# Optimization experiments

Hardware: AMD Instinct MI355X
Metric: run time of the kernel (lower is better)

Reference implementation:

```python
import jax, jax.numpy as jnp
import numpy as np

SPARSITY = 0.1  # fraction of entries kept (set to 1)


def _subnet(scores, k):
    # Mirrors GetSubnet.forward: full sort of flattened |scores|, zero the
    # lowest j = int((1-k)*n) ranks, set the rest to 1 (ties broken by sort order).
    flat = scores.ravel()
    n = flat.size
    j = int((1.0 - k) * n)  # static python int
    order = jnp.argsort(flat)  # ascending
    out = jnp.zeros((n,), dtype=scores.dtype).at[order[j:]].set(1)
    return out.reshape(scores.shape)


def setup_inputs() -> dict:
    key = jax.random.key(0)
    kA, kB = jax.random.split(key)
    # kaiming_uniform_(a=sqrt(5)) => U(-bound, bound), bound = sqrt(6/((1+5)*fan_in)) = 1/sqrt(fan_in)
    A_shape = (1024, 16384)
    B_shape = (16384, 1024)
    bA = 1.0 / np.sqrt(A_shape[1])
    bB = 1.0 / np.sqrt(B_shape[1])
    lora_A_mask = jax.random.uniform(kA, A_shape, jnp.float32, -bA, bA)
    lora_B_mask = jax.random.uniform(kB, B_shape, jnp.float32, -bB, bB)
    return {"lora_A_mask": lora_A_mask, "lora_B_mask": lora_B_mask}


def reference(lora_A_mask, lora_B_mask):
    mask_A = _subnet(jnp.abs(lora_A_mask), SPARSITY)
    mask_B = _subnet(jnp.abs(lora_B_mask), SPARSITY)
    return (mask_A, mask_B)
```

## Files before the change

kernel.cpp:

```cpp
#include <hip/hip_runtime.h>
#include <stdint.h>


#define NBINS       65536u
#define HWORDS      (2u * NBINS)
#define CCAP        65536u
#define TOTAL_WORDS 33554432u
#define RWORDS      (2u * CCAP * 2u)
#define RBASE       (TOTAL_WORDS - RWORDS)
#define SKIP_WORD   (RBASE - 16777216u)
#define SKIP_F4     (SKIP_WORD / 4u)
#define CNT(m)      (32u + (uint32_t)(m) * 16u)
#define LCAP        256u

typedef float floatx4 __attribute__((ext_vector_type(4)));

__device__ __forceinline__ void nt_store4(float4* p, float a, float b, float c, float d) {
  floatx4 v = {a, b, c, d};
  __builtin_nontemporal_store(v, reinterpret_cast<floatx4*>(p));
}

__global__ void init_k(uint32_t* __restrict__ ws, uint32_t* __restrict__ outbuf) {
  uint32_t i = blockIdx.x * blockDim.x + threadIdx.x;
  if (i < HWORDS) outbuf[i] = 0u;
  if (i < 64u) ws[i] = 0u;
}

__global__ __launch_bounds__(1024, 1) void hist_k(const float* __restrict__ A,
                                                  const float* __restrict__ B,
                                                  uint32_t* __restrict__ outbuf,
                                                  int nvec) {
  const int m = blockIdx.y;
  const float4* __restrict__ src = (const float4*)(m == 0 ? A : B);
  uint32_t* gh = outbuf + (uint32_t)m * NBINS;
  __shared__ uint32_t h[NBINS / 2];
  for (int i = threadIdx.x; i < (int)(NBINS / 2); i += blockDim.x) h[i] = 0u;
  __syncthreads();
  int idx0 = blockIdx.x * blockDim.x + threadIdx.x;
  int stride = gridDim.x * blockDim.x;
  for (int i = idx0; i < nvec; i += stride) {
    float4 f = src[i];
    const float v[4] = {f.x, f.y, f.z, f.w};
#pragma unroll
    for (int c = 0; c < 4; c++) {
      uint32_t u = __float_as_uint(v[c]) & 0x7fffffffu;
      uint32_t b = u >> 15;
      atomicAdd(&h[b >> 1], 1u << ((b & 1u) * 16u));
    }
  }
  __syncthreads();
  for (int w = threadIdx.x; w < (int)(NBINS / 2); w += blockDim.x) {
    uint32_t x = h[w];
    uint32_t c0 = x & 0xffffu, c1 = x >> 16;
    if (c0) atomicAdd(&gh[2 * w], c0);
    if (c1) atomicAdd(&gh[2 * w + 1], c1);
  }
}

__global__ __launch_bounds__(1024, 1) void scan16_k(const uint32_t* __restrict__ outbuf,
                                                    uint32_t* __restrict__ ws, uint32_t j) {
  const int m = blockIdx.x;
  const uint32_t* gh = outbuf + (uint32_t)m * NBINS;
  uint32_t* W = ws + m * 8;
  __shared__ uint32_t csum[1024];
  __shared__ uint32_t ps[1024];
  __shared__ uint32_t sChunk, sRank;
  __shared__ uint32_t bins[64];
  const int t = threadIdx.x;
  const int w = t >> 6, l = t & 63;
  for (int k = 0; k < 64; k++) {
    uint32_t v = gh[(w << 12) + (k << 6) + l];
#pragma unroll
    for (int off = 32; off; off >>= 1) v += __shfl_xor(v, off, 64);
    if (l == 0) csum[(w << 6) + k] = v;
  }
  __syncthreads();
  ps[t] = csum[t];
  __syncthreads();
  for (int off = 1; off < 1024; off <<= 1) {
    uint32_t v = (t >= off) ? ps[t - off] : 0u;
    __syncthreads();
    ps[t] += v;
    __syncthreads();
  }
  uint32_t base = (t == 0) ? 0u : ps[t - 1];
  if (j >= base && j < base + csum[t]) { sChunk = (uint32_t)t; sRank = j - base; }
  __syncthreads();
  const uint32_t chunk = sChunk, rk = sRank;
  if (t < 64) bins[t] = gh[chunk * 64u + (uint32_t)t];
  __syncthreads();
  if (t < 64) {
    uint32_t lt = 0u;
    for (int k2 = 0; k2 < t; k2++) lt += bins[k2];
    if (rk >= lt && rk < lt + bins[t]) { W[0] = chunk * 64u + (uint32_t)t; W[1] = rk - lt; }
  }
}

__global__ void mask_collect_k(const float* __restrict__ A, const float* __restrict__ B,
                               float* __restrict__ out, uint32_t* __restrict__ ws,
                               uint32_t* __restrict__ outbuf, int nvec, int n) {
  const int m = blockIdx.y;
  const float4* __restrict__ src = (const float4*)(m == 0 ? A : B);
  float4* __restrict__ dst = (float4*)(out + (size_t)m * (size_t)n);
  const uint32_t P = ws[m * 8];
  uint32_t* cand = outbuf + RBASE + (uint32_t)m * (CCAP * 2u);
  __shared__ uint32_t lbuf[2u * LCAP];
  __shared__ uint32_t ln, lbase;
  if (threadIdx.x == 0) ln = 0u;
  __syncthreads();
  const int i0 = blockIdx.x * blockDim.x + threadIdx.x;
  const int S = gridDim.x * blockDim.x;
  float4 f[4];
#pragma unroll
  for (int q = 0; q < 4; q++) {
    int i = i0 + q * S;
    if (i < nvec) f[q] = src[i];
  }
#pragma unroll
  for (int q = 0; q < 4; q++) {
    int i = i0 + q * S;
    if (i >= nvec) break;
    const float v[4] = {f[q].x, f[q].y, f[q].z, f[q].w};
    float r[4];
#pragma unroll
    for (int c = 0; c < 4; c++) {
      uint32_t u = __float_as_uint(v[c]) & 0x7fffffffu;
      uint32_t p = u >> 15;
      r[c] = (p > P) ? 1.0f : 0.0f;
      if (p == P) {
        uint32_t s = atomicAdd(&ln, 1u);
        if (s < LCAP) { lbuf[2u * s] = (uint32_t)i * 4u + (uint32_t)c; lbuf[2u * s + 1u] = u; }
      }
    }
    if (!(m == 1 && i >= (int)SKIP_F4))
      nt_store4(&dst[i], r[0], r[1], r[2], r[3]);
  }
  __syncthreads();
  uint32_t c = ln; if (c > LCAP) c = LCAP;
  if (threadIdx.x == 0 && c) lbase = atomicAdd(&ws[CNT(m)], c);
  __syncthreads();
  for (uint32_t t = threadIdx.x; t < c; t += blockDim.x) {
    uint32_t g = lbase + t;
    if (g < CCAP) { cand[2u * g] = lbuf[2u * t]; cand[2u * g + 1u] = lbuf[2u * t + 1u]; }
  }
}

__global__ __launch_bounds__(1024, 1) void select_fix_k(uint32_t* __restrict__ ws,
                                                        uint32_t* __restrict__ outbuf,
                                                        float* __restrict__ out, int n) {
  const int m = blockIdx.x;
  uint32_t* W = ws + m * 8;
  const uint32_t* cand = outbuf + RBASE + (uint32_t)m * (CCAP * 2u);
  __shared__ uint32_t h[32768];
  __shared__ uint32_t ps[1024];
  __shared__ uint32_t sT, sTarget, sC;
  __shared__ uint32_t tie_idx[1024];
  __shared__ uint32_t tie_n;
  const int t = threadIdx.x;
  uint32_t nc = ws[CNT(m)]; if (nc > CCAP) nc = CCAP;
  const uint32_t r = W[1];
  const uint32_t P = W[0];
  if (t == 0) { tie_n = 0u; sT = P << 15; sTarget = 0u; sC = 0u; }
  for (int i = t; i < 32768; i += 1024) h[i] = 0u;
  __syncthreads();
  for (uint32_t e = t; e < nc; e += 1024u)
    atomicAdd(&h[cand[2u * e + 1u] & 32767u], 1u);
  __syncthreads();
  uint32_t s = 0u;
  for (int k = 0; k < 32; k++) s += h[t * 32 + k];
  ps[t] = s;
  __syncthreads();
  for (int off = 1; off < 1024; off <<= 1) {
    uint32_t v = (t >= off) ? ps[t - off] : 0u;
    __syncthreads();
    ps[t] += v;
    __syncthreads();
  }
  uint32_t base = (t == 0) ? 0u : ps[t - 1];
  for (int k = 0; k < 32; k++) {
    uint32_t b = (uint32_t)t * 32u + (uint32_t)k;
    uint32_t c = h[b];
    if (r >= base && r < base + c) { sT = (P << 15) | b; sTarget = r - base; }
    base += c;
  }
  __syncthreads();
  const uint32_t T = sT, target = sTarget;
  for (uint32_t e = t; e < nc; e += 1024u) {
    if (cand[2u * e + 1u] == T) {
      uint32_t slot = atomicAdd(&tie_n, 1u);
      if (slot < 1024u) tie_idx[slot] = cand[2u * e];
    }
  }
  __syncthreads();
  uint32_t E2 = tie_n; if (E2 > 1024u) E2 = 1024u;
  for (uint32_t c2 = t; c2 < E2; c2 += 1024u) {
    uint32_t xi = tie_idx[c2];
    uint32_t lt = 0u;
    for (uint32_t k2 = 0; k2 < E2; k2++) lt += (tie_idx[k2] < xi) ? 1u : 0u;
    if (lt == target) sC = xi;
  }
  __syncthreads();
  if (t == 0) { W[3] = T; W[4] = sC; }
  const uint32_t C = sC;
  float* dstf = out + (size_t)m * (size_t)n;
  for (uint32_t e = t; e < nc; e += 1024u) {
    uint32_t idx = cand[2u * e];
    if (m == 1 && idx >= SKIP_WORD) continue;
    uint32_t u = cand[2u * e + 1u];
    dstf[idx] = (u > T || (u == T && idx >= C)) ? 1.0f : 0.0f;
  }
}

__global__ void fill_tail_k(const float* __restrict__ B, float* __restrict__ out,
                            const uint32_t* __restrict__ ws, int n) {
  const uint32_t* W = ws + 8;
  const uint32_t T = W[3], C = W[4];
  const float4* __restrict__ src = (const float4*)B;
  float4* __restrict__ dst = (float4*)(out + (size_t)n);
  uint32_t i = SKIP_F4 + blockIdx.x * blockDim.x + threadIdx.x;
  if (i < (uint32_t)(n / 4)) {
    float4 f = src[i];
    const float v[4] = {f.x, f.y, f.z, f.w};
    float r[4];
#pragma unroll
    for (int c = 0; c < 4; c++) {
      uint32_t u = __float_as_uint(v[c]) & 0x7fffffffu;
      uint32_t idx = i * 4u + (uint32_t)c;
      r[c] = (u > T || (u == T && idx >= C)) ? 1.0f : 0.0f;
    }
    nt_store4(&dst[i], r[0], r[1], r[2], r[3]);
  }
}

extern "C" void kernel_launch(void* const* d_in, const int* in_sizes, int n_in,
                              void* d_out, int out_size, void* d_ws, size_t ws_size,
                              hipStream_t stream) {
  const float* A = (const float*)d_in[0];
  const float* B = (const float*)d_in[1];
  float* out = (float*)d_out;
  uint32_t* ws = (uint32_t*)d_ws;
  uint32_t* outbuf = (uint32_t*)d_out;
  const int n = in_sizes[0];
  const int nvec = n / 4;
  const uint32_t j = (uint32_t)((1.0 - 0.1) * (double)n);

  init_k<<<(HWORDS + 255) / 256, 256, 0, stream>>>(ws, outbuf);
  hist_k<<<dim3(128, 2), 1024, 0, stream>>>(A, B, outbuf, nvec);
  scan16_k<<<2, 1024, 0, stream>>>(outbuf, ws, j);
  mask_collect_k<<<dim3(4096, 2), 256, 0, stream>>>(A, B, out, ws, outbuf, nvec, n);
  select_fix_k<<<2, 1024, 0, stream>>>(ws, outbuf, out, n);
  fill_tail_k<<<(n / 4 - SKIP_F4 + 255) / 256, 256, 0, stream>>>(B, out, ws, n);
}
```

Measured before the change: 413.4 us.

## Fuse radix-select pipeline into one cooperative persistent kernel with grid syncs

Replaces the six-kernel launch sequence with a single cooperative kernel that runs init, histogram, scan, mask/collect, tie-fix and tail-fill phases separated by grid.sync, sized to one 1024-thread block per CU (capped at 256 blocks). It aims to remove launch gaps and inter-kernel drains, and enlarges the per-block candidate buffer because each block now covers far more elements. The fused path uses regular stores instead of nontemporal stores, and has far fewer blocks for the bandwidth-heavy passes, so there is less memory-level parallelism. The old kernels stay as a fallback if the cooperative launch fails.

```diff
diff --git a/kernel.cpp b/kernel.cpp
--- a/kernel.cpp
+++ b/kernel.cpp
@@ -1,9 +1,11 @@
 #include <hip/hip_runtime.h>
+#include <hip/hip_cooperative_groups.h>
 #include <stdint.h>
 
+namespace cg = cooperative_groups;
+
 
 #define NBINS       65536u
-#define HWORDS      (2u * NBINS)
 #define CCAP        65536u
 #define TOTAL_WORDS 33554432u
 #define RWORDS      (2u * CCAP * 2u)
@@ -11,18 +13,233 @@
 #define SKIP_WORD   (RBASE - 16777216u)
 #define SKIP_F4     (SKIP_WORD / 4u)
 #define CNT(m)      (32u + (uint32_t)(m) * 16u)
-#define LCAP        256u
+#define TPB         1024
+#define LCAP        2048u
+#define SMW         34824
 
 typedef float floatx4 __attribute__((ext_vector_type(4)));
-
 __device__ __forceinline__ void nt_store4(float4* p, float a, float b, float c, float d) {
   floatx4 v = {a, b, c, d};
   __builtin_nontemporal_store(v, reinterpret_cast<floatx4*>(p));
 }
+__device__ __forceinline__ uint32_t agent_ld(const uint32_t* p) {
+  return __hip_atomic_load(p, __ATOMIC_RELAXED, __HIP_MEMORY_SCOPE_AGENT);
+}
+
+__global__ __launch_bounds__(1024, 1) void fused_k(
+    const float* __restrict__ A, const float* __restrict__ B,
+    float* __restrict__ out, uint32_t* __restrict__ ws,
+    int nvec, int n, uint32_t j)
+{
+  __shared__ uint32_t smem[SMW];
+  cg::grid_group grid = cg::this_grid();
+  const int nblk = (int)gridDim.x;
+  const int nbm  = nblk >> 1;
+  const int blk  = (int)blockIdx.x;
+  const int t    = (int)threadIdx.x;
+  uint32_t* outu = (uint32_t*)out;
+  const int m  = (blk >= nbm) ? 1 : 0;
+  const int bb = blk - m * nbm;
+  const int S  = nbm * TPB;
+
+  for (uint32_t i = (uint32_t)blk * TPB + t; i < 2u * NBINS; i += (uint32_t)nblk * TPB)
+    outu[i] = 0u;
+  if (blk == 0 && t < 64) ws[t] = 0u;
+  __threadfence();
+  grid.sync();
+
+  {
+    const float4* __restrict__ src = (const float4*)(m == 0 ? A : B);
+    uint32_t* gh = outu + (uint32_t)m * NBINS;
+    for (int i2 = t; i2 < 32768; i2 += TPB) smem[i2] = 0u;
+    __syncthreads();
+    for (int i = bb * TPB + t; i < nvec; i += S) {
+      float4 f = src[i];
+      const float v[4] = {f.x, f.y, f.z, f.w};
+#pragma unroll
+      for (int c = 0; c < 4; c++) {
+        uint32_t u = __float_as_uint(v[c]) & 0x7fffffffu;
+        uint32_t bin = u >> 15;
+        atomicAdd(&smem[bin >> 1], 1u << ((bin & 1u) * 16u));
+      }
+    }
+    __syncthreads();
+    for (int w = t; w < 32768; w += TPB) {
+      uint32_t x = smem[w];
+      uint32_t c0 = x & 0xffffu, c1 = x >> 16;
+      if (c0) atomicAdd(&gh[2 * w], c0);
+      if (c1) atomicAdd(&gh[2 * w + 1], c1);
+    }
+  }
+  __threadfence();
+  grid.sync();
+
+  if (blk < 2) {
+    const int mm = blk;
+    const uint32_t* gh = outu + (uint32_t)mm * NBINS;
+    uint32_t* bins = smem;
+    uint32_t* csum = smem + 32768;
+    uint32_t* ps   = smem + 33792;
+    const int w = t >> 6, l = t & 63;
+    for (int k = 0; k < 64; k++) {
+      uint32_t v = gh[(w << 12) + (k << 6) + l];
+#pragma unroll
+      for (int off = 32; off; off >>= 1) v += __shfl_xor(v, off, 64);
+      if (l == 0) csum[(w << 6) + k] = v;
+    }
+    __syncthreads();
+    ps[t] = csum[t];
+    __syncthreads();
+    for (int off = 1; off < 1024; off <<= 1) {
+      uint32_t v = (t >= off) ? ps[t - off] : 0u;
+      __syncthreads();
+      ps[t] += v;
+      __syncthreads();
+    }
+    uint32_t base = (t == 0) ? 0u : ps[t - 1];
+    if (j >= base && j < base + csum[t]) { smem[34816] = (uint32_t)t; smem[34817] = j - base; }
+    __syncthreads();
+    const uint32_t chunk = smem[34816], rk = smem[34817];
+    if (t < 64) bins[t] = gh[chunk * 64u + (uint32_t)t];
+    __syncthreads();
+    if (t < 64) {
+      uint32_t lt = 0u;
+      for (int k2 = 0; k2 < t; k2++) lt += bins[k2];
+      if (rk >= lt && rk < lt + bins[t]) {
+        ws[mm * 8] = chunk * 64u + (uint32_t)t;
+        ws[mm * 8 + 1] = rk - lt;
+      }
+    }
+  }
+  __threadfence();
+  grid.sync();
+
+  {
+    const float4* __restrict__ src = (const float4*)(m == 0 ? A : B);
+    float4* __restrict__ dst = (float4*)(out + (size_t)m * (size_t)n);
+    uint32_t* cand = outu + RBASE + (uint32_t)m * (CCAP * 2u);
+    uint32_t* lbuf = smem;
+    const uint32_t P = agent_ld(&ws[m * 8]);
+    if (t == 0) smem[34816] = 0u;
+    __syncthreads();
+    for (int i = bb * TPB + t; i < nvec; i += S) {
+      float4 f = src[i];
+      const float v[4] = {f.x, f.y, f.z, f.w};
+      float r[4];
+#pragma unroll
+      for (int c = 0; c < 4; c++) {
+        uint32_t u = __float_as_uint(v[c]) & 0x7fffffffu;
+        uint32_t p = u >> 15;
+        r[c] = (p > P) ? 1.0f : 0.0f;
+        if (p == P) {
+          uint32_t s = atomicAdd(&smem[34816], 1u);
+          if (s < LCAP) { lbuf[2u * s] = (uint32_t)i * 4u + (uint32_t)c; lbuf[2u * s + 1u] = u; }
+        }
+      }
+      if (!(m == 1 && i >= (int)SKIP_F4))
+        dst[i] = make_float4(r[0], r[1], r[2], r[3]);
+    }
+    __syncthreads();
+    uint32_t c = smem[34816]; if (c > LCAP) c = LCAP;
+    if (t == 0 && c) smem[34817] = atomicAdd(&ws[CNT(m)], c);
+    __syncthreads();
+    if (c) {
+      const uint32_t gb = smem[34817];
+      for (uint32_t e = t; e < c; e += TPB) {
+        uint32_t g = gb + e;
+        if (g < CCAP) { cand[2u * g] = lbuf[2u * e]; cand[2u * g + 1u] = lbuf[2u * e + 1u]; }
+      }
+    }
+  }
+  __threadfence();
+  grid.sync();
+
+  if (blk < 2) {
+    const int mm = blk;
+    uint32_t* W = ws + mm * 8;
+    const uint32_t* cand = outu + RBASE + (uint32_t)mm * (CCAP * 2u);
+    uint32_t* h   = smem;
+    uint32_t* ps  = smem + 32768;
+    uint32_t* tie = smem + 33792;
+    uint32_t nc = agent_ld(&ws[CNT(mm)]); if (nc > CCAP) nc = CCAP;
+    const uint32_t r = agent_ld(&W[1]);
+    const uint32_t P = agent_ld(&W[0]);
+    if (t == 0) { smem[34816] = 0u; smem[34817] = P << 15; smem[34818] = 0u; smem[34819] = 0u; }
+    for (int i2 = t; i2 < 32768; i2 += TPB) h[i2] = 0u;
+    __syncthreads();
+    for (uint32_t e = t; e < nc; e += TPB)
+      atomicAdd(&h[cand[2u * e + 1u] & 32767u], 1u);
+    __syncthreads();
+    uint32_t s = 0u;
+    for (int k = 0; k < 32; k++) s += h[t * 32 + k];
+    ps[t] = s;
+    __syncthreads();
+    for (int off = 1; off < 1024; off <<= 1) {
+      uint32_t v = (t >= off) ? ps[t - off] : 0u;
+      __syncthreads();
+      ps[t] += v;
+      __syncthreads();
+    }
+    uint32_t base = (t == 0) ? 0u : ps[t - 1];
+    for (int k = 0; k < 32; k++) {
+      uint32_t b2 = (uint32_t)t * 32u + (uint32_t)k;
+      uint32_t c2 = h[b2];
+      if (r >= base && r < base + c2) { smem[34817] = (P << 15) | b2; smem[34818] = r - base; }
+      base += c2;
+    }
+    __syncthreads();
+    const uint32_t T = smem[34817], target = smem[34818];
+    for (uint32_t e = t; e < nc; e += TPB) {
+      if (cand[2u * e + 1u] == T) {
+        uint32_t slot = atomicAdd(&smem[34816], 1u);
+        if (slot < 1024u) tie[slot] = cand[2u * e];
+      }
+    }
+    __syncthreads();
+    uint32_t E2 = smem[34816]; if (E2 > 1024u) E2 = 1024u;
+    for (uint32_t c2 = t; c2 < E2; c2 += TPB) {
+      uint32_t xi = tie[c2];
+      uint32_t lt = 0u;
+      for (uint32_t k2 = 0; k2 < E2; k2++) lt += (tie[k2] < xi) ? 1u : 0u;
+      if (lt == target) smem[34819] = xi;
+    }
+    __syncthreads();
+    if (t == 0) { W[3] = T; W[4] = smem[34819]; }
+    const uint32_t C = smem[34819];
+    float* dstf = out + (size_t)mm * (size_t)n;
+    for (uint32_t e = t; e < nc; e += TPB) {
+      uint32_t idx = cand[2u * e];
+      if (mm == 1 && idx >= SKIP_WORD) continue;
+      uint32_t u = cand[2u * e + 1u];
+      dstf[idx] = (u > T || (u == T && idx >= C)) ? 1.0f : 0.0f;
+    }
+  }
+  __threadfence();
+  grid.sync();
+
+  {
+    const uint32_t T = agent_ld(&ws[8 + 3]), C = agent_ld(&ws[8 + 4]);
+    for (uint32_t tid = (uint32_t)blk * TPB + t; tid < RWORDS / 4u; tid += (uint32_t)nblk * TPB) {
+      uint32_t i = SKIP_F4 + tid;
+      float4 f = ((const float4*)B)[i];
+      const float v[4] = {f.x, f.y, f.z, f.w};
+      float r[4];
+#pragma unroll
+      for (int c = 0; c < 4; c++) {
+        uint32_t u = __float_as_uint(v[c]) & 0x7fffffffu;
+        uint32_t idx = i * 4u + (uint32_t)c;
+        r[c] = (u > T || (u == T && idx >= C)) ? 1.0f : 0.0f;
+      }
+      ((float4*)(out + (size_t)n))[i] = make_float4(r[0], r[1], r[2], r[3]);
+    }
+  }
+}
+
+#define FLCAP 256u
 
 __global__ void init_k(uint32_t* __restrict__ ws, uint32_t* __restrict__ outbuf) {
   uint32_t i = blockIdx.x * blockDim.x + threadIdx.x;
-  if (i < HWORDS) outbuf[i] = 0u;
+  if (i < 2u * NBINS) outbuf[i] = 0u;
   if (i < 64u) ws[i] = 0u;
 }
 
@@ -104,23 +321,15 @@
   float4* __restrict__ dst = (float4*)(out + (size_t)m * (size_t)n);
   const uint32_t P = ws[m * 8];
   uint32_t* cand = outbuf + RBASE + (uint32_t)m * (CCAP * 2u);
-  __shared__ uint32_t lbuf[2u * LCAP];
+  __shared__ uint32_t lbuf[2u * FLCAP];
   __shared__ uint32_t ln, lbase;
   if (threadIdx.x == 0) ln = 0u;
   __syncthreads();
-  const int i0 = blockIdx.x * blockDim.x + threadIdx.x;
-  const int S = gridDim.x * blockDim.x;
-  float4 f[4];
-#pragma unroll
-  for (int q = 0; q < 4; q++) {
-    int i = i0 + q * S;
-    if (i < nvec) f[q] = src[i];
-  }
-#pragma unroll
-  for (int q = 0; q < 4; q++) {
-    int i = i0 + q * S;
-    if (i >= nvec) break;
-    const float v[4] = {f[q].x, f[q].y, f[q].z, f[q].w};
+  int idx0 = blockIdx.x * blockDim.x + threadIdx.x;
+  int stride = gridDim.x * blockDim.x;
+  for (int i = idx0; i < nvec; i += stride) {
+    float4 f = src[i];
+    const float v[4] = {f.x, f.y, f.z, f.w};
     float r[4];
 #pragma unroll
     for (int c = 0; c < 4; c++) {
@@ -129,14 +338,14 @@
       r[c] = (p > P) ? 1.0f : 0.0f;
       if (p == P) {
         uint32_t s = atomicAdd(&ln, 1u);
-        if (s < LCAP) { lbuf[2u * s] = (uint32_t)i * 4u + (uint32_t)c; lbuf[2u * s + 1u] = u; }
+        if (s < FLCAP) { lbuf[2u * s] = (uint32_t)i * 4u + (uint32_t)c; lbuf[2u * s + 1u] = u; }
       }
     }
     if (!(m == 1 && i >= (int)SKIP_F4))
       nt_store4(&dst[i], r[0], r[1], r[2], r[3]);
   }
   __syncthreads();
-  uint32_t c = ln; if (c > LCAP) c = LCAP;
+  uint32_t c = ln; if (c > FLCAP) c = FLCAP;
   if (threadIdx.x == 0 && c) lbase = atomicAdd(&ws[CNT(m)], c);
   __syncthreads();
   for (uint32_t t = threadIdx.x; t < c; t += blockDim.x) {
@@ -240,14 +449,32 @@
   float* out = (float*)d_out;
   uint32_t* ws = (uint32_t*)d_ws;
   uint32_t* outbuf = (uint32_t*)d_out;
-  const int n = in_sizes[0];
-  const int nvec = n / 4;
-  const uint32_t j = (uint32_t)((1.0 - 0.1) * (double)n);
-
-  init_k<<<(HWORDS + 255) / 256, 256, 0, stream>>>(ws, outbuf);
-  hist_k<<<dim3(128, 2), 1024, 0, stream>>>(A, B, outbuf, nvec);
-  scan16_k<<<2, 1024, 0, stream>>>(outbuf, ws, j);
-  mask_collect_k<<<dim3(4096, 2), 256, 0, stream>>>(A, B, out, ws, outbuf, nvec, n);
-  select_fix_k<<<2, 1024, 0, stream>>>(ws, outbuf, out, n);
-  fill_tail_k<<<(n / 4 - SKIP_F4 + 255) / 256, 256, 0, stream>>>(B, out, ws, n);
-}
+  int n = in_sizes[0];
+  int nvec = n / 4;
+  uint32_t j = (uint32_t)((1.0 - 0.1) * (double)n);
+
+  int perCU = 0, cus = 0, dev = 0;
+  (void)hipGetDevice(&dev);
+  (void)hipDeviceGetAttribute(&cus, hipDeviceAttributeMultiprocessorCount, dev);
+  hipError_t occ_err = hipOccupancyMaxActiveBlocksPerMultiprocessor(
+      &perCU, (const void*)fused_k, TPB, 0);
+  int nblk = (occ_err == hipSuccess && perCU > 0 && cus > 0) ? perCU * cus : 0;
+  if (nblk > 256) nblk = 256;
+  nblk &= ~1;
+
+  hipError_t lerr = hipErrorUnknown;
+  if (nblk >= 2) {
+    void* args[] = {(void*)&A, (void*)&B, (void*)&out, (void*)&ws,
+                    (void*)&nvec, (void*)&n, (void*)&j};
+    lerr = hipLaunchCooperativeKernel((const void*)fused_k, dim3(nblk), dim3(TPB),
+                                      args, 0, stream);
+  }
+  if (lerr != hipSuccess) {
+    init_k<<<(2u * NBINS + 255) / 256, 256, 0, stream>>>(ws, outbuf);
+    hist_k<<<dim3(128, 2), 1024, 0, stream>>>(A, B, outbuf, nvec);
+    scan16_k<<<2, 1024, 0, stream>>>(outbuf, ws, j);
+    mask_collect_k<<<dim3(4096, 2), 256, 0, stream>>>(A, B, out, ws, outbuf, nvec, n);
+    select_fix_k<<<2, 1024, 0, stream>>>(ws, outbuf, out, n);
+    fill_tail_k<<<(n / 4 - SKIP_F4 + 255) / 256, 256, 0, stream>>>(B, out, ws, n);
+  }
+}
```

Result: slower. 772.6 us (+86.9%).
